# Kernel optimization log

Hardware: AMD Instinct MI355X
Metric: run time of the kernel (lower is better)

Reference implementation:

```python
import jax, jax.numpy as jnp
import numpy as np

B, N_C, Y_DIM = 8, 2048, 8
GRID_RES = 128
GRID_MIN, GRID_MAX = -1.0, 1.0
SIGMA0 = 0.1


def _make_grid_points():
    x = jnp.linspace(GRID_MIN, GRID_MAX, GRID_RES, dtype=jnp.float32)
    y = jnp.linspace(GRID_MIN, GRID_MAX, GRID_RES, dtype=jnp.float32)
    gy, gx = jnp.meshgrid(y, x, indexing='ij')
    return jnp.stack([gx, gy], axis=-1).reshape(1, -1, 2)  # (1, R*R, 2)


def setup_inputs() -> dict:
    key = jax.random.key(0)
    k1, k2 = jax.random.split(key)
    x_c = jax.random.uniform(k1, (B, N_C, 2), dtype=jnp.float32, minval=GRID_MIN, maxval=GRID_MAX)
    y_c = jax.random.normal(k2, (B, N_C, Y_DIM), dtype=jnp.float32)
    grid_points = _make_grid_points()
    sigma = jnp.asarray(SIGMA0, dtype=jnp.float32)
    return {"x_c": x_c, "y_c": y_c, "grid_points": grid_points, "sigma": sigma}


def reference(x_c, y_c, grid_points, sigma):
    g = grid_points[0]                                    # (M, 2)
    xn = jnp.sum(x_c * x_c, axis=-1)                      # (B, N)
    gn = jnp.sum(g * g, axis=-1)                          # (M,)
    cross = jnp.einsum('bnd,md->bnm', x_c, g)             # (B, N, M)
    d2 = xn[:, :, None] + gn[None, None, :] - 2.0 * cross # (B, N, M)
    weights = jnp.exp(-0.5 * d2 / (sigma * sigma))        # (B, N, M)
    density = jnp.sum(weights, axis=1)                    # (B, M)
    signal = jnp.einsum('bny,bnm->bym', y_c, weights)     # (B, Y, M)
    normalized = signal / (density[:, None, :] + 1e-5)
    out = jnp.concatenate([density[:, None, :], normalized], axis=1)  # (B, 1+Y, M)
    return out.reshape(x_c.shape[0], -1, GRID_RES, GRID_RES)
```

## Files before the change

### kernel.cpp

```cpp
#include <hip/hip_runtime.h>


typedef float  f32x4 __attribute__((ext_vector_type(4)));
typedef __fp16 half8  __attribute__((ext_vector_type(8)));
typedef __fp16 half2t __attribute__((ext_vector_type(2)));

constexpr int B_  = 8;
constexpr int NC  = 2048;
constexpr int M_  = 128 * 128;
constexpr int BLK = 512;
constexpr int KW  = 256;
constexpr int LDHY = NC + 8;

constexpr int OFF_SXT = 0;
constexpr int OFF_SYT = OFF_SXT + NC * 4;
constexpr int OFF_SYS = OFF_SYT + NC * 4;
constexpr int OFF_SG  = OFF_SYS + 8 * LDHY * 2;
constexpr int POOL_B  = OFF_SG + 32 * 4;
constexpr int SLOT_F = 9 * 256;

__global__ __launch_bounds__(BLK) void rbf_sep(
    const float* __restrict__ x_c,
    const float* __restrict__ y_c,
    const float* __restrict__ gp,
    const float* __restrict__ sigma_p,
    float* __restrict__ out)
{
    __shared__ __align__(16) char pool[POOL_B];
    float*  sxt = (float*)(pool + OFF_SXT);
    float*  syt = (float*)(pool + OFF_SYT);
    __fp16* sys = (__fp16*)(pool + OFF_SYS);
    float*  sg  = (float*)(pool + OFF_SG);

    const int tid  = (int)threadIdx.x;
    const int lane = tid & 63;
    const int w    = tid >> 6;
    const int q    = lane >> 4;
    const int cl   = lane & 15;

    const int bid = blockIdx.x;
    const int b   = bid >> 6;
    const int myg = (bid >> 3) & 7;
    const int mxg = bid & 7;
    const int my0 = myg * 16;
    const int mx0 = mxg * 16;

    const float sigma = sigma_p[0];
    const float s = __builtin_sqrtf(0.72134752044448170f) / sigma;

    if (tid < 16)      sg[tid] = s * gp[(my0 + tid) * 256 + 1];
    else if (tid < 32) sg[tid] = s * gp[(mx0 + (tid - 16)) * 2];

    const float2* xb = (const float2*)x_c + (size_t)b * NC;
    const float4* yb = (const float4*)y_c + (size_t)b * NC * 2;
    for (int it = tid; it < NC; it += BLK) {
        const float2 v = xb[it];
        sxt[it] = s * v.x;
        syt[it] = s * v.y;
        const float4 y0 = yb[(size_t)it * 2];
        const float4 y1 = yb[(size_t)it * 2 + 1];
        __fp16* yw = sys + it;
        yw[0 * LDHY] = (__fp16)y0.x;
        yw[1 * LDHY] = (__fp16)y0.y;
        yw[2 * LDHY] = (__fp16)y0.z;
        yw[3 * LDHY] = (__fp16)y0.w;
        yw[4 * LDHY] = (__fp16)y1.x;
        yw[5 * LDHY] = (__fp16)y1.y;
        yw[6 * LDHY] = (__fp16)y1.z;
        yw[7 * LDHY] = (__fp16)y1.w;
    }
    __syncthreads();

    const float sgy_r = sg[cl];
    const float sgx_r = sg[16 + cl];

    f32x4 acc[9];
#pragma unroll
    for (int c = 0; c < 9; ++c) acc[c] = (f32x4)0.0f;

    const int kbase = w * KW;
#pragma unroll 2
    for (int ks = 0; ks < KW / 32; ++ks) {
        const int kq = kbase + ks * 32 + q * 8;

        const f32x4 ya0 = *(const f32x4*)(syt + kq);
        const f32x4 ya1 = *(const f32x4*)(syt + kq + 4);
        const f32x4 ye0 = ya0 - sgy_r, ye1 = ya1 - sgy_r;
        const f32x4 ym0 = ye0 * ye0,   ym1 = ye1 * ye1;
        const half2t a0 = __builtin_amdgcn_cvt_pkrtz(
            __builtin_amdgcn_exp2f(-ym0.x), __builtin_amdgcn_exp2f(-ym0.y));
        const half2t a1 = __builtin_amdgcn_cvt_pkrtz(
            __builtin_amdgcn_exp2f(-ym0.z), __builtin_amdgcn_exp2f(-ym0.w));
        const half2t a2 = __builtin_amdgcn_cvt_pkrtz(
            __builtin_amdgcn_exp2f(-ym1.x), __builtin_amdgcn_exp2f(-ym1.y));
        const half2t a3 = __builtin_amdgcn_cvt_pkrtz(
            __builtin_amdgcn_exp2f(-ym1.z), __builtin_amdgcn_exp2f(-ym1.w));
        const half8 af = (half8){a0.x, a0.y, a1.x, a1.y, a2.x, a2.y, a3.x, a3.y};

        const f32x4 xa0 = *(const f32x4*)(sxt + kq);
        const f32x4 xa1 = *(const f32x4*)(sxt + kq + 4);
        const f32x4 xe0 = xa0 - sgx_r, xe1 = xa1 - sgx_r;
        const f32x4 xm0 = xe0 * xe0,   xm1 = xe1 * xe1;
        const half2t b0 = __builtin_amdgcn_cvt_pkrtz(
            __builtin_amdgcn_exp2f(-xm0.x), __builtin_amdgcn_exp2f(-xm0.y));
        const half2t b1 = __builtin_amdgcn_cvt_pkrtz(
            __builtin_amdgcn_exp2f(-xm0.z), __builtin_amdgcn_exp2f(-xm0.w));
        const half2t b2 = __builtin_amdgcn_cvt_pkrtz(
            __builtin_amdgcn_exp2f(-xm1.x), __builtin_amdgcn_exp2f(-xm1.y));
        const half2t b3 = __builtin_amdgcn_cvt_pkrtz(
            __builtin_amdgcn_exp2f(-xm1.z), __builtin_amdgcn_exp2f(-xm1.w));
        const half8 bx = (half8){b0.x, b0.y, b1.x, b1.y, b2.x, b2.y, b3.x, b3.y};

        acc[0] = __builtin_amdgcn_mfma_f32_16x16x32_f16(af, bx, acc[0], 0, 0, 0);
        const __fp16* yp = sys + kq;
#pragma unroll
        for (int c = 0; c < 8; ++c) {
            const half8 yf = *(const half8*)(yp + c * LDHY);
            acc[c + 1] = __builtin_amdgcn_mfma_f32_16x16x32_f16(af, bx * yf, acc[c + 1], 0, 0, 0);
        }
    }

    __syncthreads();
    float* slots = (float*)pool;
    if (w >= 4) {
        float* rb = slots + (w - 4) * SLOT_F;
#pragma unroll
        for (int c = 0; c < 9; ++c)
#pragma unroll
            for (int r = 0; r < 4; ++r)
                rb[c * 256 + (q * 4 + r) * 16 + cl] = acc[c][r];
    }
    __syncthreads();
    if (w < 4) {
        float* rb = slots + w * SLOT_F;
#pragma unroll
        for (int c = 0; c < 9; ++c)
#pragma unroll
            for (int r = 0; r < 4; ++r) {
                const int idx = c * 256 + (q * 4 + r) * 16 + cl;
                rb[idx] = rb[idx] + acc[c][r];
            }
    }
    __syncthreads();

    if (tid < 256) {
        float* ob = out + (size_t)b * 9 * M_;
        const int my = tid >> 4, mx = tid & 15;
        const size_t mo = (size_t)(my0 + my) * 128 + mx0 + mx;
        float v[9];
#pragma unroll
        for (int c = 0; c < 9; ++c) {
            const int idx = c * 256 + tid;
            v[c] = (slots[idx] + slots[SLOT_F + idx]) +
                   (slots[2 * SLOT_F + idx] + slots[3 * SLOT_F + idx]);
        }
        const float inv = __builtin_amdgcn_rcpf(v[0] + 1e-5f);
        ob[mo] = v[0];
#pragma unroll
        for (int c = 1; c < 9; ++c)
            ob[(size_t)c * M_ + mo] = v[c] * inv;
    }
}

extern "C" void kernel_launch(void* const* d_in, const int* in_sizes, int n_in,
                              void* d_out, int out_size, void* d_ws, size_t ws_size,
                              hipStream_t stream) {
    const float* x_c   = (const float*)d_in[0];
    const float* y_c   = (const float*)d_in[1];
    const float* gp    = (const float*)d_in[2];
    const float* sigma = (const float*)d_in[3];
    float* out = (float*)d_out;

    dim3 grid(B_ * 64);
    dim3 block(BLK);
    rbf_sep<<<grid, block, 0, stream>>>(x_c, y_c, gp, sigma, out);
}
```

Before: 17.74 us.

## Compute two 16-row tiles per block to reuse x-factor and y products

Each block now covers a 32x16 grid tile instead of 16x16, computing two A fragments per step that share the x-direction factor and the bx*y products. The block grows to 1024 threads with half the K per wave, and the grid is halved. Staging of x_c/y_c into shared memory now happens half as often, and the x exponentials and half-precision multiplies are amortised over two MFMAs. The reduction is widened to 8 slots, and the final output is written with vectorised float4 stores. The costs are twice the accumulator registers per thread, a larger shared pool (about 147KB), and only 256 blocks, which may reduce occupancy.

```diff
diff --git a/kernel.cpp b/kernel.cpp
--- a/kernel.cpp
+++ b/kernel.cpp
@@ -8,16 +8,16 @@
 constexpr int B_  = 8;
 constexpr int NC  = 2048;
 constexpr int M_  = 128 * 128;
-constexpr int BLK = 512;
-constexpr int KW  = 256;
+constexpr int BLK = 1024;
+constexpr int KW  = 128;
 constexpr int LDHY = NC + 8;
 
 constexpr int OFF_SXT = 0;
 constexpr int OFF_SYT = OFF_SXT + NC * 4;
 constexpr int OFF_SYS = OFF_SYT + NC * 4;
 constexpr int OFF_SG  = OFF_SYS + 8 * LDHY * 2;
-constexpr int POOL_B  = OFF_SG + 32 * 4;
-constexpr int SLOT_F = 9 * 256;
+constexpr int SLOT_F  = 2 * 9 * 256;
+constexpr int POOL_B  = 8 * SLOT_F * 4;
 
 __global__ __launch_bounds__(BLK) void rbf_sep(
     const float* __restrict__ x_c,
@@ -39,17 +39,17 @@
     const int cl   = lane & 15;
 
     const int bid = blockIdx.x;
-    const int b   = bid >> 6;
-    const int myg = (bid >> 3) & 7;
+    const int b   = bid >> 5;
+    const int myg = (bid >> 3) & 3;
     const int mxg = bid & 7;
-    const int my0 = myg * 16;
+    const int my0 = myg * 32;
     const int mx0 = mxg * 16;
 
     const float sigma = sigma_p[0];
     const float s = __builtin_sqrtf(0.72134752044448170f) / sigma;
 
-    if (tid < 16)      sg[tid] = s * gp[(my0 + tid) * 256 + 1];
-    else if (tid < 32) sg[tid] = s * gp[(mx0 + (tid - 16)) * 2];
+    if (tid < 32)      sg[tid] = s * gp[(my0 + tid) * 256 + 1];
+    else if (tid < 48) sg[tid] = s * gp[(mx0 + (tid - 32)) * 2];
 
     const float2* xb = (const float2*)x_c + (size_t)b * NC;
     const float4* yb = (const float4*)y_c + (size_t)b * NC * 2;
@@ -71,12 +71,15 @@
     }
     __syncthreads();
 
-    const float sgy_r = sg[cl];
-    const float sgx_r = sg[16 + cl];
-
-    f32x4 acc[9];
-#pragma unroll
-    for (int c = 0; c < 9; ++c) acc[c] = (f32x4)0.0f;
+    const float sgy0 = sg[cl];
+    const float sgy1 = sg[16 + cl];
+    const float sgxr = sg[32 + cl];
+
+    f32x4 acc[2][9];
+#pragma unroll
+    for (int t = 0; t < 2; ++t)
+#pragma unroll
+        for (int c = 0; c < 9; ++c) acc[t][c] = (f32x4)0.0f;
 
     const int kbase = w * KW;
 #pragma unroll 2
@@ -85,21 +88,34 @@
 
         const f32x4 ya0 = *(const f32x4*)(syt + kq);
         const f32x4 ya1 = *(const f32x4*)(syt + kq + 4);
-        const f32x4 ye0 = ya0 - sgy_r, ye1 = ya1 - sgy_r;
-        const f32x4 ym0 = ye0 * ye0,   ym1 = ye1 * ye1;
-        const half2t a0 = __builtin_amdgcn_cvt_pkrtz(
-            __builtin_amdgcn_exp2f(-ym0.x), __builtin_amdgcn_exp2f(-ym0.y));
-        const half2t a1 = __builtin_amdgcn_cvt_pkrtz(
-            __builtin_amdgcn_exp2f(-ym0.z), __builtin_amdgcn_exp2f(-ym0.w));
-        const half2t a2 = __builtin_amdgcn_cvt_pkrtz(
-            __builtin_amdgcn_exp2f(-ym1.x), __builtin_amdgcn_exp2f(-ym1.y));
-        const half2t a3 = __builtin_amdgcn_cvt_pkrtz(
-            __builtin_amdgcn_exp2f(-ym1.z), __builtin_amdgcn_exp2f(-ym1.w));
-        const half8 af = (half8){a0.x, a0.y, a1.x, a1.y, a2.x, a2.y, a3.x, a3.y};
-
         const f32x4 xa0 = *(const f32x4*)(sxt + kq);
         const f32x4 xa1 = *(const f32x4*)(sxt + kq + 4);
-        const f32x4 xe0 = xa0 - sgx_r, xe1 = xa1 - sgx_r;
+
+        const f32x4 y0e0 = ya0 - sgy0, y0e1 = ya1 - sgy0;
+        const f32x4 y0m0 = y0e0 * y0e0, y0m1 = y0e1 * y0e1;
+        const half2t p00 = __builtin_amdgcn_cvt_pkrtz(
+            __builtin_amdgcn_exp2f(-y0m0.x), __builtin_amdgcn_exp2f(-y0m0.y));
+        const half2t p01 = __builtin_amdgcn_cvt_pkrtz(
+            __builtin_amdgcn_exp2f(-y0m0.z), __builtin_amdgcn_exp2f(-y0m0.w));
+        const half2t p02 = __builtin_amdgcn_cvt_pkrtz(
+            __builtin_amdgcn_exp2f(-y0m1.x), __builtin_amdgcn_exp2f(-y0m1.y));
+        const half2t p03 = __builtin_amdgcn_cvt_pkrtz(
+            __builtin_amdgcn_exp2f(-y0m1.z), __builtin_amdgcn_exp2f(-y0m1.w));
+        const half8 af0 = (half8){p00.x, p00.y, p01.x, p01.y, p02.x, p02.y, p03.x, p03.y};
+
+        const f32x4 y1e0 = ya0 - sgy1, y1e1 = ya1 - sgy1;
+        const f32x4 y1m0 = y1e0 * y1e0, y1m1 = y1e1 * y1e1;
+        const half2t p10 = __builtin_amdgcn_cvt_pkrtz(
+            __builtin_amdgcn_exp2f(-y1m0.x), __builtin_amdgcn_exp2f(-y1m0.y));
+        const half2t p11 = __builtin_amdgcn_cvt_pkrtz(
+            __builtin_amdgcn_exp2f(-y1m0.z), __builtin_amdgcn_exp2f(-y1m0.w));
+        const half2t p12 = __builtin_amdgcn_cvt_pkrtz(
+            __builtin_amdgcn_exp2f(-y1m1.x), __builtin_amdgcn_exp2f(-y1m1.y));
+        const half2t p13 = __builtin_amdgcn_cvt_pkrtz(
+            __builtin_amdgcn_exp2f(-y1m1.z), __builtin_amdgcn_exp2f(-y1m1.w));
+        const half8 af1 = (half8){p10.x, p10.y, p11.x, p11.y, p12.x, p12.y, p13.x, p13.y};
+
+        const f32x4 xe0 = xa0 - sgxr, xe1 = xa1 - sgxr;
         const f32x4 xm0 = xe0 * xe0,   xm1 = xe1 * xe1;
         const half2t b0 = __builtin_amdgcn_cvt_pkrtz(
             __builtin_amdgcn_exp2f(-xm0.x), __builtin_amdgcn_exp2f(-xm0.y));
@@ -111,54 +127,72 @@
             __builtin_amdgcn_exp2f(-xm1.z), __builtin_amdgcn_exp2f(-xm1.w));
         const half8 bx = (half8){b0.x, b0.y, b1.x, b1.y, b2.x, b2.y, b3.x, b3.y};
 
-        acc[0] = __builtin_amdgcn_mfma_f32_16x16x32_f16(af, bx, acc[0], 0, 0, 0);
+        acc[0][0] = __builtin_amdgcn_mfma_f32_16x16x32_f16(af0, bx, acc[0][0], 0, 0, 0);
+        acc[1][0] = __builtin_amdgcn_mfma_f32_16x16x32_f16(af1, bx, acc[1][0], 0, 0, 0);
         const __fp16* yp = sys + kq;
 #pragma unroll
         for (int c = 0; c < 8; ++c) {
-            const half8 yf = *(const half8*)(yp + c * LDHY);
-            acc[c + 1] = __builtin_amdgcn_mfma_f32_16x16x32_f16(af, bx * yf, acc[c + 1], 0, 0, 0);
+            const half8 yf  = *(const half8*)(yp + c * LDHY);
+            const half8 bxy = bx * yf;
+            acc[0][c + 1] = __builtin_amdgcn_mfma_f32_16x16x32_f16(af0, bxy, acc[0][c + 1], 0, 0, 0);
+            acc[1][c + 1] = __builtin_amdgcn_mfma_f32_16x16x32_f16(af1, bxy, acc[1][c + 1], 0, 0, 0);
         }
     }
 
     __syncthreads();
     float* slots = (float*)pool;
-    if (w >= 4) {
-        float* rb = slots + (w - 4) * SLOT_F;
-#pragma unroll
-        for (int c = 0; c < 9; ++c)
-#pragma unroll
-            for (int r = 0; r < 4; ++r)
-                rb[c * 256 + (q * 4 + r) * 16 + cl] = acc[c][r];
-    }
-    __syncthreads();
-    if (w < 4) {
+    if (w >= 8) {
+        float* rb = slots + (w - 8) * SLOT_F;
+#pragma unroll
+        for (int t = 0; t < 2; ++t)
+#pragma unroll
+            for (int c = 0; c < 9; ++c)
+#pragma unroll
+                for (int r = 0; r < 4; ++r)
+                    rb[t * 2304 + c * 256 + (q * 4 + r) * 16 + cl] = acc[t][c][r];
+    }
+    __syncthreads();
+    if (w < 8) {
         float* rb = slots + w * SLOT_F;
 #pragma unroll
-        for (int c = 0; c < 9; ++c)
-#pragma unroll
-            for (int r = 0; r < 4; ++r) {
-                const int idx = c * 256 + (q * 4 + r) * 16 + cl;
-                rb[idx] = rb[idx] + acc[c][r];
-            }
-    }
-    __syncthreads();
-
-    if (tid < 256) {
-        float* ob = out + (size_t)b * 9 * M_;
-        const int my = tid >> 4, mx = tid & 15;
-        const size_t mo = (size_t)(my0 + my) * 128 + mx0 + mx;
-        float v[9];
-#pragma unroll
-        for (int c = 0; c < 9; ++c) {
-            const int idx = c * 256 + tid;
-            v[c] = (slots[idx] + slots[SLOT_F + idx]) +
-                   (slots[2 * SLOT_F + idx] + slots[3 * SLOT_F + idx]);
+        for (int t = 0; t < 2; ++t)
+#pragma unroll
+            for (int c = 0; c < 9; ++c)
+#pragma unroll
+                for (int r = 0; r < 4; ++r) {
+                    const int idx = t * 2304 + c * 256 + (q * 4 + r) * 16 + cl;
+                    rb[idx] = rb[idx] + acc[t][c][r];
+                }
+    }
+    __syncthreads();
+
+    float* ob = out + (size_t)b * 9 * M_;
+    for (int it = tid; it < 1152; it += BLK) {
+        const int t  = it / 576;
+        const int rr = it % 576;
+        const int c  = rr >> 6;
+        const int my = (rr & 63) >> 2;
+        const int xq = rr & 3;
+        const int base  = t * 2304 + c * 256 + my * 16 + xq * 4;
+        const int dbase = t * 2304 +           my * 16 + xq * 4;
+
+        #define SUM8(off) ( (*(const f32x4*)(slots + 0*SLOT_F + (off)) + *(const f32x4*)(slots + 1*SLOT_F + (off))) \
+                          + (*(const f32x4*)(slots + 2*SLOT_F + (off)) + *(const f32x4*)(slots + 3*SLOT_F + (off))) \
+                          + ((*(const f32x4*)(slots + 4*SLOT_F + (off)) + *(const f32x4*)(slots + 5*SLOT_F + (off))) \
+                          +  (*(const f32x4*)(slots + 6*SLOT_F + (off)) + *(const f32x4*)(slots + 7*SLOT_F + (off)))) )
+        const f32x4 v = SUM8(base);
+        f32x4 o;
+        if (c == 0) {
+            o = v;
+        } else {
+            const f32x4 d = SUM8(dbase);
+            o.x = v.x * __builtin_amdgcn_rcpf(d.x + 1e-5f);
+            o.y = v.y * __builtin_amdgcn_rcpf(d.y + 1e-5f);
+            o.z = v.z * __builtin_amdgcn_rcpf(d.z + 1e-5f);
+            o.w = v.w * __builtin_amdgcn_rcpf(d.w + 1e-5f);
         }
-        const float inv = __builtin_amdgcn_rcpf(v[0] + 1e-5f);
-        ob[mo] = v[0];
-#pragma unroll
-        for (int c = 1; c < 9; ++c)
-            ob[(size_t)c * M_ + mo] = v[c] * inv;
+        #undef SUM8
+        *(f32x4*)(ob + (size_t)c * M_ + (size_t)(my0 + t * 16 + my) * 128 + mx0 + xq * 4) = o;
     }
 }
 
@@ -171,7 +205,7 @@
     const float* sigma = (const float*)d_in[3];
     float* out = (float*)d_out;
 
-    dim3 grid(B_ * 64);
+    dim3 grid(B_ * 32);
     dim3 block(BLK);
     rbf_sep<<<grid, block, 0, stream>>>(x_c, y_c, gp, sigma, out);
 }
```

After: 17.92 us. Within noise of the previous version (+1.0%).

## Split staging into two double-buffered chunks overlapping global loads with compute

Applied to the files above, without the earlier changes.

Stages the context points in two chunks of 1024 held in separate shared-memory buffers. The second chunk's global loads are issued before the first chunk is computed and written to LDS afterwards, so load latency is hidden behind MFMA and exp work. Staging loads are also widened to float4 with paired half2 stores. The cost is more registers held across the first compute phase and a larger shared-memory footprint. The second buffer is written without a barrier after the first chunk's reads, which is safe only because it is a separate buffer.

```diff
diff --git a/kernel.cpp b/kernel.cpp
--- a/kernel.cpp
+++ b/kernel.cpp
@@ -9,15 +9,16 @@
 constexpr int NC  = 2048;
 constexpr int M_  = 128 * 128;
 constexpr int BLK = 512;
-constexpr int KW  = 256;
-constexpr int LDHY = NC + 8;
+constexpr int CH  = 1024;
+constexpr int LDHY = CH + 8;
 
 constexpr int OFF_SXT = 0;
-constexpr int OFF_SYT = OFF_SXT + NC * 4;
-constexpr int OFF_SYS = OFF_SYT + NC * 4;
-constexpr int OFF_SG  = OFF_SYS + 8 * LDHY * 2;
-constexpr int POOL_B  = OFF_SG + 32 * 4;
-constexpr int SLOT_F = 9 * 256;
+constexpr int OFF_SYT = OFF_SXT + CH * 4;
+constexpr int OFF_SYS = OFF_SYT + CH * 4;
+constexpr int BUF_B   = OFF_SYS + 8 * LDHY * 2;
+constexpr int OFF_SG  = 2 * BUF_B;
+constexpr int POOL_B  = OFF_SG + 48 * 4;
+constexpr int SLOT_F  = 9 * 256;
 
 __global__ __launch_bounds__(BLK) void rbf_sep(
     const float* __restrict__ x_c,
@@ -27,10 +28,7 @@
     float* __restrict__ out)
 {
     __shared__ __align__(16) char pool[POOL_B];
-    float*  sxt = (float*)(pool + OFF_SXT);
-    float*  syt = (float*)(pool + OFF_SYT);
-    __fp16* sys = (__fp16*)(pool + OFF_SYS);
-    float*  sg  = (float*)(pool + OFF_SG);
+    float* sg = (float*)(pool + OFF_SG);
 
     const int tid  = (int)threadIdx.x;
     const int lane = tid & 63;
@@ -51,74 +49,110 @@
     if (tid < 16)      sg[tid] = s * gp[(my0 + tid) * 256 + 1];
     else if (tid < 32) sg[tid] = s * gp[(mx0 + (tid - 16)) * 2];
 
-    const float2* xb = (const float2*)x_c + (size_t)b * NC;
-    const float4* yb = (const float4*)y_c + (size_t)b * NC * 2;
-    for (int it = tid; it < NC; it += BLK) {
-        const float2 v = xb[it];
-        sxt[it] = s * v.x;
-        syt[it] = s * v.y;
-        const float4 y0 = yb[(size_t)it * 2];
-        const float4 y1 = yb[(size_t)it * 2 + 1];
-        __fp16* yw = sys + it;
-        yw[0 * LDHY] = (__fp16)y0.x;
-        yw[1 * LDHY] = (__fp16)y0.y;
-        yw[2 * LDHY] = (__fp16)y0.z;
-        yw[3 * LDHY] = (__fp16)y0.w;
-        yw[4 * LDHY] = (__fp16)y1.x;
-        yw[5 * LDHY] = (__fp16)y1.y;
-        yw[6 * LDHY] = (__fp16)y1.z;
-        yw[7 * LDHY] = (__fp16)y1.w;
+    const float4* xb4 = (const float4*)(x_c + (size_t)b * NC * 2);
+    const float4* yb4 = (const float4*)(y_c + (size_t)b * NC * 8);
+
+    float4 xv0 = xb4[tid];
+    float4 ya0g = yb4[4 * tid + 0];
+    float4 yb0g = yb4[4 * tid + 1];
+    float4 yc0g = yb4[4 * tid + 2];
+    float4 yd0g = yb4[4 * tid + 3];
+
+    {
+        float*  sxtb = (float*)(pool + OFF_SXT);
+        float*  sytb = (float*)(pool + OFF_SYT);
+        __fp16* sysb = (__fp16*)(pool + OFF_SYS);
+        *(float2*)(sxtb + 2 * tid) = (float2){s * xv0.x, s * xv0.z};
+        *(float2*)(sytb + 2 * tid) = (float2){s * xv0.y, s * xv0.w};
+        *(half2t*)(sysb + 0 * LDHY + 2 * tid) = (half2t){(__fp16)ya0g.x, (__fp16)yc0g.x};
+        *(half2t*)(sysb + 1 * LDHY + 2 * tid) = (half2t){(__fp16)ya0g.y, (__fp16)yc0g.y};
+        *(half2t*)(sysb + 2 * LDHY + 2 * tid) = (half2t){(__fp16)ya0g.z, (__fp16)yc0g.z};
+        *(half2t*)(sysb + 3 * LDHY + 2 * tid) = (half2t){(__fp16)ya0g.w, (__fp16)yc0g.w};
+        *(half2t*)(sysb + 4 * LDHY + 2 * tid) = (half2t){(__fp16)yb0g.x, (__fp16)yd0g.x};
+        *(half2t*)(sysb + 5 * LDHY + 2 * tid) = (half2t){(__fp16)yb0g.y, (__fp16)yd0g.y};
+        *(half2t*)(sysb + 6 * LDHY + 2 * tid) = (half2t){(__fp16)yb0g.z, (__fp16)yd0g.z};
+        *(half2t*)(sysb + 7 * LDHY + 2 * tid) = (half2t){(__fp16)yb0g.w, (__fp16)yd0g.w};
     }
     __syncthreads();
 
     const float sgy_r = sg[cl];
     const float sgx_r = sg[16 + cl];
 
+    float4 xv1 = xb4[512 + tid];
+    float4 ya1g = yb4[2048 + 4 * tid + 0];
+    float4 yb1g = yb4[2048 + 4 * tid + 1];
+    float4 yc1g = yb4[2048 + 4 * tid + 2];
+    float4 yd1g = yb4[2048 + 4 * tid + 3];
+
     f32x4 acc[9];
 #pragma unroll
     for (int c = 0; c < 9; ++c) acc[c] = (f32x4)0.0f;
 
-    const int kbase = w * KW;
-#pragma unroll 2
-    for (int ks = 0; ks < KW / 32; ++ks) {
-        const int kq = kbase + ks * 32 + q * 8;
-
-        const f32x4 ya0 = *(const f32x4*)(syt + kq);
-        const f32x4 ya1 = *(const f32x4*)(syt + kq + 4);
-        const f32x4 ye0 = ya0 - sgy_r, ye1 = ya1 - sgy_r;
-        const f32x4 ym0 = ye0 * ye0,   ym1 = ye1 * ye1;
-        const half2t a0 = __builtin_amdgcn_cvt_pkrtz(
-            __builtin_amdgcn_exp2f(-ym0.x), __builtin_amdgcn_exp2f(-ym0.y));
-        const half2t a1 = __builtin_amdgcn_cvt_pkrtz(
-            __builtin_amdgcn_exp2f(-ym0.z), __builtin_amdgcn_exp2f(-ym0.w));
-        const half2t a2 = __builtin_amdgcn_cvt_pkrtz(
-            __builtin_amdgcn_exp2f(-ym1.x), __builtin_amdgcn_exp2f(-ym1.y));
-        const half2t a3 = __builtin_amdgcn_cvt_pkrtz(
-            __builtin_amdgcn_exp2f(-ym1.z), __builtin_amdgcn_exp2f(-ym1.w));
-        const half8 af = (half8){a0.x, a0.y, a1.x, a1.y, a2.x, a2.y, a3.x, a3.y};
-
-        const f32x4 xa0 = *(const f32x4*)(sxt + kq);
-        const f32x4 xa1 = *(const f32x4*)(sxt + kq + 4);
-        const f32x4 xe0 = xa0 - sgx_r, xe1 = xa1 - sgx_r;
-        const f32x4 xm0 = xe0 * xe0,   xm1 = xe1 * xe1;
-        const half2t b0 = __builtin_amdgcn_cvt_pkrtz(
-            __builtin_amdgcn_exp2f(-xm0.x), __builtin_amdgcn_exp2f(-xm0.y));
-        const half2t b1 = __builtin_amdgcn_cvt_pkrtz(
-            __builtin_amdgcn_exp2f(-xm0.z), __builtin_amdgcn_exp2f(-xm0.w));
-        const half2t b2 = __builtin_amdgcn_cvt_pkrtz(
-            __builtin_amdgcn_exp2f(-xm1.x), __builtin_amdgcn_exp2f(-xm1.y));
-        const half2t b3 = __builtin_amdgcn_cvt_pkrtz(
-            __builtin_amdgcn_exp2f(-xm1.z), __builtin_amdgcn_exp2f(-xm1.w));
-        const half8 bx = (half8){b0.x, b0.y, b1.x, b1.y, b2.x, b2.y, b3.x, b3.y};
-
-        acc[0] = __builtin_amdgcn_mfma_f32_16x16x32_f16(af, bx, acc[0], 0, 0, 0);
-        const __fp16* yp = sys + kq;
-#pragma unroll
-        for (int c = 0; c < 8; ++c) {
-            const half8 yf = *(const half8*)(yp + c * LDHY);
-            acc[c + 1] = __builtin_amdgcn_mfma_f32_16x16x32_f16(af, bx * yf, acc[c + 1], 0, 0, 0);
-        }
-    }
+#define COMPUTE_CHUNK(BUFOFF)                                                     \
+    {                                                                             \
+        const float*  sxtb = (const float*)(pool + (BUFOFF) + OFF_SXT);           \
+        const float*  sytb = (const float*)(pool + (BUFOFF) + OFF_SYT);           \
+        const __fp16* sysb = (const __fp16*)(pool + (BUFOFF) + OFF_SYS);          \
+        _Pragma("unroll")                                                         \
+        for (int ks = 0; ks < 4; ++ks) {                                          \
+            const int kq = w * 128 + ks * 32 + q * 8;                             \
+            const f32x4 ya0 = *(const f32x4*)(sytb + kq);                         \
+            const f32x4 ya1 = *(const f32x4*)(sytb + kq + 4);                     \
+            const f32x4 xa0 = *(const f32x4*)(sxtb + kq);                         \
+            const f32x4 xa1 = *(const f32x4*)(sxtb + kq + 4);                     \
+            const f32x4 ye0 = ya0 - sgy_r, ye1 = ya1 - sgy_r;                     \
+            const f32x4 ym0 = ye0 * ye0,   ym1 = ye1 * ye1;                       \
+            const half2t a0 = __builtin_amdgcn_cvt_pkrtz(                         \
+                __builtin_amdgcn_exp2f(-ym0.x), __builtin_amdgcn_exp2f(-ym0.y));  \
+            const half2t a1 = __builtin_amdgcn_cvt_pkrtz(                         \
+                __builtin_amdgcn_exp2f(-ym0.z), __builtin_amdgcn_exp2f(-ym0.w));  \
+            const half2t a2 = __builtin_amdgcn_cvt_pkrtz(                         \
+                __builtin_amdgcn_exp2f(-ym1.x), __builtin_amdgcn_exp2f(-ym1.y));  \
+            const half2t a3 = __builtin_amdgcn_cvt_pkrtz(                         \
+                __builtin_amdgcn_exp2f(-ym1.z), __builtin_amdgcn_exp2f(-ym1.w));  \
+            const half8 af = (half8){a0.x, a0.y, a1.x, a1.y, a2.x, a2.y, a3.x, a3.y}; \
+            const f32x4 xe0 = xa0 - sgx_r, xe1 = xa1 - sgx_r;                     \
+            const f32x4 xm0 = xe0 * xe0,   xm1 = xe1 * xe1;                       \
+            const half2t b0 = __builtin_amdgcn_cvt_pkrtz(                         \
+                __builtin_amdgcn_exp2f(-xm0.x), __builtin_amdgcn_exp2f(-xm0.y));  \
+            const half2t b1 = __builtin_amdgcn_cvt_pkrtz(                         \
+                __builtin_amdgcn_exp2f(-xm0.z), __builtin_amdgcn_exp2f(-xm0.w));  \
+            const half2t b2 = __builtin_amdgcn_cvt_pkrtz(                         \
+                __builtin_amdgcn_exp2f(-xm1.x), __builtin_amdgcn_exp2f(-xm1.y));  \
+            const half2t b3 = __builtin_amdgcn_cvt_pkrtz(                         \
+                __builtin_amdgcn_exp2f(-xm1.z), __builtin_amdgcn_exp2f(-xm1.w));  \
+            const half8 bx = (half8){b0.x, b0.y, b1.x, b1.y, b2.x, b2.y, b3.x, b3.y}; \
+            acc[0] = __builtin_amdgcn_mfma_f32_16x16x32_f16(af, bx, acc[0], 0, 0, 0); \
+            const __fp16* yp = sysb + kq;                                         \
+            _Pragma("unroll")                                                     \
+            for (int c = 0; c < 8; ++c) {                                         \
+                const half8 yf = *(const half8*)(yp + c * LDHY);                  \
+                acc[c + 1] = __builtin_amdgcn_mfma_f32_16x16x32_f16(af, bx * yf, acc[c + 1], 0, 0, 0); \
+            }                                                                     \
+        }                                                                         \
+    }
+
+    COMPUTE_CHUNK(0)
+
+    {
+        float*  sxtb = (float*)(pool + BUF_B + OFF_SXT);
+        float*  sytb = (float*)(pool + BUF_B + OFF_SYT);
+        __fp16* sysb = (__fp16*)(pool + BUF_B + OFF_SYS);
+        *(float2*)(sxtb + 2 * tid) = (float2){s * xv1.x, s * xv1.z};
+        *(float2*)(sytb + 2 * tid) = (float2){s * xv1.y, s * xv1.w};
+        *(half2t*)(sysb + 0 * LDHY + 2 * tid) = (half2t){(__fp16)ya1g.x, (__fp16)yc1g.x};
+        *(half2t*)(sysb + 1 * LDHY + 2 * tid) = (half2t){(__fp16)ya1g.y, (__fp16)yc1g.y};
+        *(half2t*)(sysb + 2 * LDHY + 2 * tid) = (half2t){(__fp16)ya1g.z, (__fp16)yc1g.z};
+        *(half2t*)(sysb + 3 * LDHY + 2 * tid) = (half2t){(__fp16)ya1g.w, (__fp16)yc1g.w};
+        *(half2t*)(sysb + 4 * LDHY + 2 * tid) = (half2t){(__fp16)yb1g.x, (__fp16)yd1g.x};
+        *(half2t*)(sysb + 5 * LDHY + 2 * tid) = (half2t){(__fp16)yb1g.y, (__fp16)yd1g.y};
+        *(half2t*)(sysb + 6 * LDHY + 2 * tid) = (half2t){(__fp16)yb1g.z, (__fp16)yd1g.z};
+        *(half2t*)(sysb + 7 * LDHY + 2 * tid) = (half2t){(__fp16)yb1g.w, (__fp16)yd1g.w};
+    }
+    __syncthreads();
+
+    COMPUTE_CHUNK(BUF_B)
+#undef COMPUTE_CHUNK
 
     __syncthreads();
     float* slots = (float*)pool;
```

New measurement: 17.65 us. No clear change (-0.5%).
